# Performance work log

Hardware: AMD Instinct MI355X
Metric: run time of the kernel (lower is better)

The kernel has to match this reference:

```python
import jax, jax.numpy as jnp
import numpy as np
from math import factorial

N_NODES = 20000
N_EDGES = 80000
NUM_GRAPHS = 64
NUM_NEIGHBORS = 3.8
POOL_NODES = 4.0  # num_nodes=4 constant in source forward

# ---------------- real Wigner 3j (e3nn-style, Frobenius norm 1) ----------------

def _w3j_complex(j1, j2, j3, m1, m2, m3):
    if m1 + m2 + m3 != 0:
        return 0.0
    t1 = j2 - m1 - j3; t2 = j1 + m2 - j3; t3 = j1 + j2 - j3
    t4 = j1 - m1; t5 = j2 + m2
    tmin = max(0, t1, t2); tmax = min(t3, t4, t5)
    if tmin > tmax:
        return 0.0
    s = 0.0
    for t in range(tmin, tmax + 1):
        s += (-1.0) ** t / (factorial(t) * factorial(t - t1) * factorial(t - t2)
                            * factorial(t3 - t) * factorial(t4 - t) * factorial(t5 - t))
    tri = (factorial(j1 + j2 - j3) * factorial(j1 - j2 + j3) * factorial(-j1 + j2 + j3)
           / factorial(j1 + j2 + j3 + 1))
    norm = np.sqrt(tri * factorial(j1 + m1) * factorial(j1 - m1) * factorial(j2 + m2)
                   * factorial(j2 - m2) * factorial(j3 + m3) * factorial(j3 - m3))
    return (-1.0) ** (j1 - j2 - m3) * norm * s


def _real_basis(l):
    U = np.zeros((2 * l + 1, 2 * l + 1), dtype=np.complex128)
    U[l, l] = 1.0
    for m in range(1, l + 1):
        U[l + m, l + m] = (-1) ** m / np.sqrt(2.0)
        U[l + m, l - m] = 1.0 / np.sqrt(2.0)
        U[l - m, l - m] = 1j / np.sqrt(2.0)
        U[l - m, l + m] = -1j * (-1) ** m / np.sqrt(2.0)
    return U

_W3J_CACHE = {}

def w3j(l1, l2, l3):
    key = (l1, l2, l3)
    if key not in _W3J_CACHE:
        C = np.zeros((2 * l1 + 1, 2 * l2 + 1, 2 * l3 + 1), dtype=np.complex128)
        for m1 in range(-l1, l1 + 1):
            for m2 in range(-l2, l2 + 1):
                m3 = -(m1 + m2)
                if -l3 <= m3 <= l3:
                    C[m1 + l1, m2 + l2, m3 + l3] = _w3j_complex(l1, l2, l3, m1, m2, m3)
        C = np.einsum('ia,jb,kc,abc->ijk', _real_basis(l1), _real_basis(l2), _real_basis(l3), C)
        C = np.real((-1j) ** (l1 + l2 + l3) * C)
        _W3J_CACHE[key] = jnp.asarray(C, dtype=jnp.float32)
    return _W3J_CACHE[key]

# ---------------- irreps bookkeeping ----------------
SH        = [(1, 0, 1), (1, 1, -1), (1, 2, 1), (1, 3, -1)]            # 1x0e+1x1o+1x2e+1x3o (dim 16)
GATE1_IN  = [(16,0,1),(16,0,-1),(8,0,1),(8,0,-1),(8,0,1),(8,0,-1),(16,1,-1),(16,1,1)]  # dim 160
GATE1_OUT = [(16,0,1),(16,0,1),(16,1,-1),(16,1,1)]                     # dim 128
GATE2_IN  = [(16,0,1),(16,0,-1),(6,0,1),(6,0,-1),(6,0,1),(6,0,-1),(12,1,-1),(12,1,1)]  # dim 128
GATE2_OUT = [(16,0,1),(16,0,1),(12,1,-1),(12,1,1)]                     # dim 104
OUT_FINAL = [(1, 0, 1)]


def slices(irreps):
    out = []; o = 0
    for m, l, p in irreps:
        d = m * (2 * l + 1); out.append((o, o + d)); o += d
    return out


def tp_paths(ir1, ir2, iro):
    paths = []
    for i1, (m1, l1, p1) in enumerate(ir1):
        for i2, (m2, l2, p2) in enumerate(ir2):
            for io, (mo, lo, po) in enumerate(iro):
                if po == p1 * p2 and abs(l1 - l2) <= lo <= l1 + l2:
                    paths.append((i1, i2, io))
    fan = [0] * len(iro)
    for i1, i2, io in paths:
        fan[io] += ir1[i1][0] * ir2[i2][0]
    numel = sum(ir1[i1][0] * ir2[i2][0] * iro[io][0] for i1, i2, io in paths)
    return paths, fan, numel


def tensor_product(x1, x2, weights, ir1, ir2, iro):
    # FullyConnectedTensorProduct, component norm, element path normalization
    paths, fan, numel = tp_paths(ir1, ir2, iro)
    s1, s2 = slices(ir1), slices(ir2)
    E = x1.shape[0]
    out_parts = [jnp.zeros((E, m * (2 * l + 1)), x1.dtype) for m, l, p in iro]
    wofs = 0
    for i1, i2, io in paths:
        m1, l1, _ = ir1[i1]; m2, l2, _ = ir2[i2]; mo, lo, _ = iro[io]
        n = m1 * m2 * mo
        w = weights[:, wofs:wofs + n].reshape(E, m1, m2, mo); wofs += n
        a = x1[:, s1[i1][0]:s1[i1][1]].reshape(E, m1, 2 * l1 + 1)
        b = x2[:, s2[i2][0]:s2[i2][1]].reshape(E, m2, 2 * l2 + 1)
        C = w3j(l1, l2, lo)
        pw = np.sqrt((2 * lo + 1) / fan[io])
        seg = jnp.einsum('eui,evj,ijk,euvw->ewk', a, b, C, w) * pw
        out_parts[io] = out_parts[io] + seg.reshape(E, mo * (2 * lo + 1))
    return jnp.concatenate(out_parts, axis=1)

# ---------------- activations / gate ----------------
_xs = np.linspace(-8.0, 8.0, 100001)
_pdf = np.exp(-0.5 * _xs ** 2) / np.sqrt(2 * np.pi)
TANH_NORM = float(1.0 / np.sqrt(np.sum(np.tanh(_xs) ** 2 * _pdf) * (_xs[1] - _xs[0])))
SQRT2 = float(np.sqrt(2.0))
ACT = {'relu': lambda t: jnp.maximum(t, 0.0) * SQRT2,
       'abs':  lambda t: jnp.abs(t),
       'tanh': lambda t: jnp.tanh(t) * TANH_NORM}


def gate_fn(x, scalars, gates, gated):
    o = 0; outs = []
    for m, a in scalars:
        outs.append(ACT[a](x[:, o:o + m])); o += m
    gv = []
    for m, a in gates:
        gv.append(ACT[a](x[:, o:o + m])); o += m
    g = jnp.concatenate(gv, axis=-1)
    gi = 0
    for m, l in gated:
        d = 2 * l + 1
        feat = x[:, o:o + m * d].reshape(-1, m, d)
        outs.append((feat * g[:, gi:gi + m, None]).reshape(-1, m * d))
        o += m * d; gi += m
    return jnp.concatenate(outs, axis=-1)

# ---------------- edge features ----------------

def sh_component(v):
    # real spherical harmonics l=0..3, 'component' normalization, unit input
    x, y, z = v[:, 0], v[:, 1], v[:, 2]
    s3, s5, s15 = np.sqrt(3.0), np.sqrt(5.0), np.sqrt(15.0)
    s7, s42, s70, s105 = np.sqrt(7.0), np.sqrt(42.0), np.sqrt(70.0), np.sqrt(105.0)
    Y0 = jnp.ones_like(x)[:, None]
    Y1 = jnp.stack([s3 * y, s3 * z, s3 * x], -1)
    Y2 = jnp.stack([s15 * x * y, s15 * y * z, 0.5 * s5 * (3 * z * z - 1.0),
                    s15 * x * z, 0.5 * s15 * (x * x - y * y)], -1)
    Y3 = jnp.stack([0.25 * s70 * y * (3 * x * x - y * y), s105 * x * y * z,
                    0.25 * s42 * y * (5 * z * z - 1.0), 0.5 * s7 * z * (5 * z * z - 3.0),
                    0.25 * s42 * x * (5 * z * z - 1.0), 0.5 * s105 * z * (x * x - y * y),
                    0.25 * s70 * x * (x * x - 3 * y * y)], -1)
    return jnp.concatenate([Y0, Y1, Y2, Y3], -1)  # [E,16]


def soft_one_hot(r):
    # soft_one_hot_linspace(start=0.5,end=2.5,number=3,basis='smooth_finite',cutoff=True)
    values = np.linspace(0.5, 2.5, 5)[1:-1]
    step = values[1] - values[0]
    diff = (r[:, None] - values) / step
    def f(u):
        return jnp.where(u > 0, jnp.exp(-1.0 / jnp.where(u > 0, u, 1.0)), 0.0)
    y = 1.14136 * np.exp(2.0) * f(diff + 1.0) * f(1.0 - diff)
    return y * np.sqrt(3.0)


def fc(x, w1, w2):
    # e3nn FullyConnectedNet([3,256,numel], relu)
    h = jnp.maximum(x @ (w1 / np.sqrt(w1.shape[0])), 0.0) * SQRT2
    return h @ (w2 / np.sqrt(w2.shape[0]))


def convolution(node_feats, edge_src, edge_dst, edge_attr, edge_scalars, w1, w2, ir_in, ir_out, n_nodes):
    weight = fc(edge_scalars, w1, w2)                                   # [E, numel]
    ef = tensor_product(node_feats[edge_src], edge_attr, weight, ir_in, SH, ir_out)
    return jax.ops.segment_sum(ef, edge_dst, num_segments=n_nodes) / np.sqrt(NUM_NEIGHBORS)


def _forward(pos, w1_1, w2_1, w1_2, w2_2, w1_3, w2_3, edge_src, edge_dst, batch):
    N = pos.shape[0]
    vec = pos[edge_src] - pos[edge_dst]
    r = jnp.sqrt(jnp.sum(vec * vec, axis=1) + 1e-12)
    unit = vec / r[:, None]
    edge_attr = sh_component(unit)
    edge_scalars = soft_one_hot(r)
    x = jax.ops.segment_sum(edge_attr, edge_dst, num_segments=N) / np.sqrt(NUM_NEIGHBORS)
    x = convolution(x, edge_src, edge_dst, edge_attr, edge_scalars, w1_1, w2_1, SH, GATE1_IN, N)
    x = gate_fn(x, [(16, 'relu'), (16, 'abs')], [(8, 'relu'), (8, 'tanh'), (8, 'relu'), (8, 'tanh')], [(16, 1), (16, 1)])
    x = convolution(x, edge_src, edge_dst, edge_attr, edge_scalars, w1_2, w2_2, GATE1_OUT, GATE2_IN, N)
    x = gate_fn(x, [(16, 'relu'), (16, 'abs')], [(6, 'relu'), (6, 'tanh'), (6, 'relu'), (6, 'tanh')], [(12, 1), (12, 1)])
    x = convolution(x, edge_src, edge_dst, edge_attr, edge_scalars, w1_3, w2_3, GATE2_OUT, OUT_FINAL, N)
    x = jax.ops.segment_sum(x, batch, num_segments=NUM_GRAPHS) / np.sqrt(POOL_NODES)
    return jax.nn.sigmoid(x)


def setup_inputs():
    key = jax.random.key(0)
    ks = jax.random.split(key, 10)
    pos = jax.random.normal(ks[0], (N_NODES, 3), jnp.float32) * 1.5
    edge_src = jax.random.randint(ks[1], (N_EDGES,), 0, N_NODES)
    edge_dst = jax.random.randint(ks[2], (N_EDGES,), 0, N_NODES)
    batch = jnp.sort(jax.random.randint(ks[3], (N_NODES,), 0, NUM_GRAPHS))
    _, _, n1 = tp_paths(SH, SH, GATE1_IN)
    _, _, n2 = tp_paths(GATE1_OUT, SH, GATE2_IN)
    _, _, n3 = tp_paths(GATE2_OUT, SH, OUT_FINAL)
    w1_1 = jax.random.normal(ks[4], (3, 256), jnp.float32)
    w2_1 = jax.random.normal(ks[5], (256, n1), jnp.float32)
    w1_2 = jax.random.normal(ks[6], (3, 256), jnp.float32)
    w2_2 = jax.random.normal(ks[7], (256, n2), jnp.float32)
    w1_3 = jax.random.normal(ks[8], (3, 256), jnp.float32)
    w2_3 = jax.random.normal(ks[9], (256, n3), jnp.float32)
    return {'pos': pos, 'w1_1': w1_1, 'w2_1': w2_1, 'w1_2': w1_2, 'w2_2': w2_2,
            'w1_3': w1_3, 'w2_3': w2_3, 'edge_src': edge_src, 'edge_dst': edge_dst, 'batch': batch}


def reference(pos, w1_1, w2_1, w1_2, w2_2, w1_3, w2_3, edge_src, edge_dst, batch):
    return _forward(pos, w1_1, w2_1, w1_2, w2_2, w1_3, w2_3, edge_src, edge_dst, batch)
```

## Files before the change

kernel.cpp:

```cpp
#include <hip/hip_runtime.h>
#include <math.h>

#define NNODE 20000
#define NEDGE 80000
#define NGRAPH 64

#define OFF_TANH  656
#define OFF_CNT   660
#define OFF_GSUM  664
#define OFF_HIST  7680
#define OFF_OFFS  9728
#define OFF_CUR   11784
#define OFF_EATTR 14336
#define OFF_RBUF  1294336
#define OFF_EINFO 1374336
#define OFF_X0    1694336
#define OFF_Y1    2014336
#define OFF_Y2    5214336
#define OFF_X1    7774336
#define OFF_X2    10334336
#define OFF_TAB   12414336

#define T000 0
#define T110 1
#define T220 10
#define T330 35
#define T011 84
#define T101 93
#define T111 102
#define T121 129
#define T211 174
#define T231 219
#define T321 324
#define T221 429
#define T331 504

#define INV_SQRT_NEIGH 0.5129891760425771f
#define SQRT2F 1.4142135623730951f

struct TabD { int l1,l2,l3,off; };
constexpr TabD HTABS[13] = {
  {0,0,0,T000},{1,1,0,T110},{2,2,0,T220},{3,3,0,T330},
  {0,1,1,T011},{1,0,1,T101},{1,1,1,T111},{1,2,1,T121},
  {2,1,1,T211},{2,3,1,T231},{3,2,1,T321},{2,2,1,T221},{3,3,1,T331}
};

struct CoreD { short a_off, b_off; short l1,l2,l3; short tab; short coff; short m1; };
struct PathD { short core; short wofs, wend, ooff; short mo, lo; float pw; };

constexpr CoreD HCORES1[13] = {
  {0,0, 0,0,0, T000, 0, 1},
  {0,1, 0,1,1, T011, 1, 1},
  {1,0, 1,0,1, T101, 4, 1},
  {1,1, 1,1,0, T110, 7, 1},
  {1,1, 1,1,1, T111, 8, 1},
  {1,4, 1,2,1, T121, 11, 1},
  {4,1, 2,1,1, T211, 14, 1},
  {4,4, 2,2,0, T220, 17, 1},
  {4,4, 2,2,1, T221, 18, 1},
  {4,9, 2,3,1, T231, 21, 1},
  {9,4, 3,2,1, T321, 24, 1},
  {9,9, 3,3,0, T330, 27, 1},
  {9,9, 3,3,1, T331, 28, 1}
};
#define PWR 0.7071067811865476f
constexpr PathD HPATHS1[21] = {
  {0,  0, 16,  0,16,0,0.5f},
  {0, 16, 24, 32, 8,0,0.5f},
  {0, 24, 32, 48, 8,0,0.5f},
  {1, 32, 48, 64,16,1,PWR},
  {2, 48, 64, 64,16,1,PWR},
  {3, 64, 80,  0,16,0,0.5f},
  {3, 80, 88, 32, 8,0,0.5f},
  {3, 88, 96, 48, 8,0,0.5f},
  {4, 96,112,112,16,1,1.0f},
  {5,112,128, 64,16,1,PWR},
  {6,128,144, 64,16,1,PWR},
  {7,144,160,  0,16,0,0.5f},
  {7,160,168, 32, 8,0,0.5f},
  {7,168,176, 48, 8,0,0.5f},
  {8,176,192,112,16,1,1.0f},
  {9,192,208, 64,16,1,PWR},
  {10,208,224,64,16,1,PWR},
  {11,224,240, 0,16,0,0.5f},
  {11,240,248,32, 8,0,0.5f},
  {11,248,256,48, 8,0,0.5f},
  {12,256,272,112,16,1,1.0f}
};

constexpr CoreD HCORES2[12] = {
  {0,0,  0,0,0, T000, 0,   16},
  {0,1,  0,1,1, T011, 16,  16},
  {16,0, 0,0,0, T000, 64,  16},
  {16,1, 0,1,1, T011, 80,  16},
  {32,0, 1,0,1, T101, 128, 16},
  {32,1, 1,1,0, T110, 176, 16},
  {32,1, 1,1,1, T111, 192, 16},
  {32,4, 1,2,1, T121, 240, 16},
  {80,0, 1,0,1, T101, 288, 16},
  {80,1, 1,1,0, T110, 336, 16},
  {80,1, 1,1,1, T111, 352, 16},
  {80,4, 1,2,1, T121, 400, 16}
};
#define PA 0.14433756729740643f
#define PB 0.25f
#define PC 0.19364916731037085f
constexpr PathD HPATHS2[20] = {
  {0,   0, 256,  0,16,0,PA},
  {0, 256, 352, 32, 6,0,PA},
  {0, 352, 448, 44, 6,0,PA},
  {1, 448, 640, 56,12,1,PC},
  {2, 640, 896,  0,16,0,PA},
  {2, 896, 992, 32, 6,0,PA},
  {2, 992,1088, 44, 6,0,PA},
  {3,1088,1280, 56,12,1,PC},
  {4,1280,1472, 56,12,1,PC},
  {5,1472,1728,  0,16,0,PA},
  {5,1728,1824, 32, 6,0,PA},
  {5,1824,1920, 44, 6,0,PA},
  {6,1920,2112, 92,12,1,PB},
  {7,2112,2304, 56,12,1,PC},
  {8,2304,2496, 92,12,1,PB},
  {9,2496,2752, 16,16,0,PB},
  {9,2752,2848, 38, 6,0,PB},
  {9,2848,2944, 50, 6,0,PB},
  {10,2944,3136,56,12,1,PC},
  {11,3136,3328,92,12,1,PB}
};

constexpr CoreD HCORES3[3] = {
  {0,0,  0,0,0, T000, 0,  16},
  {16,0, 0,0,0, T000, 16, 16},
  {32,1, 1,1,0, T110, 32, 12}
};
#define PD 0.15075567228888181f
constexpr PathD HPATHS3[3] = {
  {0, 0,16, 0,1,0,PD},
  {1,16,32, 0,1,0,PD},
  {2,32,44, 0,1,0,PD}
};

constexpr double FACT[9] = {1.0,1.0,2.0,6.0,24.0,120.0,720.0,5040.0,40320.0};

constexpr double csqrt_(double x){
  if(x<=0.0) return 0.0;
  double g = (x<1.0)? 1.0 : x;
  for(int i=0;i<40;i++) g = 0.5*(g + x/g);
  return g;
}

constexpr double cw3j_(int j1,int j2,int j3,int m1,int m2,int m3){
  if(m1+m2+m3!=0) return 0.0;
  int t1=j2-m1-j3, t2=j1+m2-j3, t3=j1+j2-j3, t4=j1-m1, t5=j2+m2;
  int tmin=t1>0?t1:0; if(t2>tmin) tmin=t2;
  int tmax=t3<t4?t3:t4; if(t5<tmax) tmax=t5;
  if(tmin>tmax) return 0.0;
  double s=0.0;
  for(int t=tmin;t<=tmax;++t){
    double d=FACT[t]*FACT[t-t1]*FACT[t-t2]*FACT[t3-t]*FACT[t4-t]*FACT[t5-t];
    s += ((t&1)? -1.0:1.0)/d;
  }
  double tri=FACT[j1+j2-j3]*FACT[j1-j2+j3]*FACT[-j1+j2+j3]/FACT[j1+j2+j3+1];
  double nrm=csqrt_(tri*FACT[j1+m1]*FACT[j1-m1]*FACT[j2+m2]*FACT[j2-m2]*FACT[j3+m3]*FACT[j3-m3]);
  return (((j1-j2-m3)&1)? -1.0:1.0)*nrm*s;
}

constexpr int curow_(int l,int i,int* a,double* re,double* im){
  const double is2=0.7071067811865475;
  int m=i-l;
  if(m==0){ a[0]=l; re[0]=1.0; im[0]=0.0; return 1; }
  if(m>0){
    a[0]=l+m; re[0]=((m&1)? -is2:is2); im[0]=0.0;
    a[1]=l-m; re[1]=is2; im[1]=0.0; return 2;
  }
  int mm=-m;
  a[0]=l-mm; re[0]=0.0; im[0]=is2;
  a[1]=l+mm; re[1]=0.0; im[1]=((mm&1)? is2:-is2);
  return 2;
}

constexpr float cw3j_elem_(int l1,int l2,int l3,int i,int j,int k){
  int aa[2]={0,0},bb[2]={0,0},cc[2]={0,0};
  double ar[2]={0,0},ai[2]={0,0},br[2]={0,0},bi[2]={0,0},cr[2]={0,0},ci[2]={0,0};
  int na=curow_(l1,i,aa,ar,ai);
  int nb=curow_(l2,j,bb,br,bi);
  int nc=curow_(l3,k,cc,cr,ci);
  double accr=0.0, acci=0.0;
  for(int x=0;x<na;x++)for(int y=0;y<nb;y++)for(int w=0;w<nc;w++){
    double wv=cw3j_(l1,l2,l3, aa[x]-l1, bb[y]-l2, cc[w]-l3);
    if(wv==0.0) continue;
    double pr=ar[x]*br[y]-ai[x]*bi[y];
    double pi=ar[x]*bi[y]+ai[x]*br[y];
    double qr=pr*cr[w]-pi*ci[w];
    double qi=pr*ci[w]+pi*cr[w];
    accr+=qr*wv; acci+=qi*wv;
  }
  int Lm=(l1+l2+l3)&3;
  double res = (Lm==0)? accr : (Lm==1)? acci : (Lm==2)? -accr : -acci;
  return (float)res;
}

struct WApart { float v[429]; };
constexpr WApart gen_wa_(){
  WApart o{};
  for(int t=0;t<11;t++){
    int l1=HTABS[t].l1,l2=HTABS[t].l2,l3=HTABS[t].l3;
    int n2=2*l2+1,n3=2*l3+1;
    int tot=(2*l1+1)*n2*n3;
    for(int z=0;z<tot;z++){
      int i=z/(n2*n3), j=(z/n3)%n2, k=z%n3;
      o.v[HTABS[t].off+z]=cw3j_elem_(l1,l2,l3,i,j,k);
    }
  }
  return o;
}
struct WBpart { float v[222]; };
constexpr WBpart gen_wb_(){
  WBpart o{};
  for(int t=11;t<13;t++){
    int l1=HTABS[t].l1,l2=HTABS[t].l2,l3=HTABS[t].l3;
    int n2=2*l2+1,n3=2*l3+1;
    int tot=(2*l1+1)*n2*n3;
    for(int z=0;z<tot;z++){
      int i=z/(n2*n3), j=(z/n3)%n2, k=z%n3;
      o.v[HTABS[t].off-429+z]=cw3j_elem_(l1,l2,l3,i,j,k);
    }
  }
  return o;
}
constexpr WApart WAC = gen_wa_();
constexpr WBpart WBC = gen_wb_();
struct W3Full { float v[651]; };
constexpr W3Full gen_wfull_(){
  W3Full f{};
  for(int i=0;i<429;i++) f.v[i]=WAC.v[i];
  for(int i=0;i<222;i++) f.v[429+i]=WBC.v[i];
  return f;
}
__constant__ W3Full W3JC = gen_wfull_();

template<int NW> struct PwArr { float v[NW]; };
template<int NW,int NP>
constexpr PwArr<NW> gen_pw_(const PathD (&P)[NP]){
  PwArr<NW> a{};
  for(int p=0;p<NP;p++)
    for(int j=P[p].wofs;j<P[p].wend;j++) a.v[j]=P[p].pw;
  return a;
}
__constant__ PwArr<272>  PWC1 = gen_pw_<272>(HPATHS1);
__constant__ PwArr<3328> PWC2 = gen_pw_<3328>(HPATHS2);
__constant__ PwArr<44>   PWC3 = gen_pw_<44>(HPATHS3);

struct OutSeg { int mult, l; };
constexpr OutSeg OSEG1[8] = {{16,0},{16,0},{8,0},{8,0},{8,0},{8,0},{16,1},{16,1}};
constexpr OutSeg OSEG2[8] = {{16,0},{16,0},{6,0},{6,0},{6,0},{6,0},{12,1},{12,1}};
constexpr OutSeg OSEG3[1] = {{1,0}};

struct Ent2 { int jb, cb, nu; };
template<int NCOL,int NENT,int NW> struct ColMetaT {
  int cidx[NCOL+1];
  int obase[NCOL];
  int n3c[NCOL];
  Ent2 ent[NENT];
  int newj[NW];
};

template<int NCOL,int NENT,int NW,int NSEG,int NP,int NC>
constexpr ColMetaT<NCOL,NENT,NW> gen_colmeta_(const OutSeg (&S)[NSEG], const PathD (&P)[NP], const CoreD (&C)[NC]){
  ColMetaT<NCOL,NENT,NW> m{};
  int col=0, cnt=0, o=0, nb=0;
  for(int s=0;s<NSEG;s++){
    int n3=2*S[s].l+1;
    for(int wc=0;wc<S[s].mult;wc++){
      m.cidx[col]=cnt;
      int ob=o+wc*n3;
      m.obase[col]=ob;
      m.n3c[col]=n3;
      for(int p=0;p<NP;p++){
        PathD pd=P[p];
        int pn3=2*pd.lo+1;
        if(pn3!=n3) continue;
        int rel=ob-pd.ooff;
        if(rel<0||rel>=pd.mo*pn3) continue;
        int w=rel/pn3;
        CoreD cd=C[pd.core];
        int m1=cd.m1;
        m.ent[cnt]=Ent2{nb,(int)cd.coff,m1};
        for(int u=0;u<m1;u++) m.newj[pd.wofs + w + u*pd.mo]=nb+u;
        nb+=m1;
        cnt++;
      }
      col++;
    }
    o+=S[s].mult*n3;
  }
  m.cidx[col]=cnt;
  return m;
}

__constant__ ColMetaT<96,272,272>  CMETA1 = gen_colmeta_<96,272,272>(OSEG1, HPATHS1, HCORES1);
__constant__ ColMetaT<80,208,3328> CMETA2 = gen_colmeta_<80,208,3328>(OSEG2, HPATHS2, HCORES2);
__constant__ ColMetaT< 1,  3,  44> CMETA3 = gen_colmeta_< 1,  3,  44>(OSEG3, HPATHS3, HCORES3);

struct CItem { short aoff, boff, n1, n2, cofs, jstep, woff, pad; };
struct CArr1 { CItem it[31]; };
constexpr CArr1 gen_c1_(){
  CArr1 a{}; int s=0;
  for(int cn=0;cn<13;cn++){
    CoreD cd=HCORES1[cn];
    int n1=2*cd.l1+1,n2=2*cd.l2+1,n3=2*cd.l3+1;
    for(int k=0;k<n3;k++){
      a.it[s]=CItem{cd.a_off,cd.b_off,(short)n1,(short)n2,(short)(cd.tab+k),(short)n3,(short)(cd.coff+k),0};
      s++;
    }
  }
  return a;
}
__constant__ CArr1 CIT1 = gen_c1_();

struct Fam { short b_off, tab, n1, n2, n3, goff; };
constexpr Fam GF2[6]={
  {0,T000,1,1,1,0},{1,T011,1,3,3,1},{0,T101,3,1,3,4},
  {1,T110,3,3,1,13},{1,T111,3,3,3,16},{4,T121,3,5,3,25}};
constexpr Fam GF3[2]={{0,T000,1,1,1,0},{1,T110,3,3,1,1}};
struct CoreG { short fam,a_off,m1,coff; };
constexpr CoreG CG2[12]={
  {0,0,16,0},{1,0,16,16},{0,16,16,64},{1,16,16,80},
  {2,32,16,128},{3,32,16,176},{4,32,16,192},{5,32,16,240},
  {2,80,16,288},{3,80,16,336},{4,80,16,352},{5,80,16,400}};
constexpr CoreG CG3[3]={{0,0,16,0},{0,16,16,16},{1,32,12,32}};

struct GItem { short boff, cofs, n2, jstep; };
template<int NG> struct GArrT { GItem it[NG]; };
template<int NG,int NF>
constexpr GArrT<NG> gen_g_(const Fam (&F)[NF]){
  GArrT<NG> a{}; int s=0;
  for(int f=0;f<NF;f++){
    for(int i=0;i<F[f].n1;i++)for(int k=0;k<F[f].n3;k++){
      a.it[s]=GItem{F[f].b_off,(short)(F[f].tab + i*F[f].n2*F[f].n3 + k),F[f].n2,F[f].n3};
      s++;
    }
  }
  return a;
}
__constant__ GArrT<34> GIT2=gen_g_<34>(GF2);
__constant__ GArrT<4>  GIT3=gen_g_<4>(GF3);

struct OItem { short aoff, gofs, n1, n3, woff, pad; };
template<int NO> struct OArrT { OItem it[NO]; };
template<int NO,int NC,int NF>
constexpr OArrT<NO> gen_o_(const CoreG (&C)[NC], const Fam (&F)[NF]){
  OArrT<NO> a{}; int s=0;
  for(int cn=0;cn<NC;cn++){
    Fam f=F[C[cn].fam];
    for(int k=0;k<f.n3;k++)for(int u=0;u<C[cn].m1;u++){
      a.it[s]=OItem{(short)(C[cn].a_off+u*f.n1),(short)(f.goff+k),f.n1,f.n3,
                    (short)(C[cn].coff+k*C[cn].m1+u),0};
      s++;
    }
  }
  return a;
}
__constant__ OArrT<448> OIT2=gen_o_<448,12,6>(CG2,GF2);
__constant__ OArrT<44>  OIT3=gen_o_<44,3,2>(CG3,GF3);

template<int CNT,int N3,int NCOLS>
__device__ __forceinline__ void apply1_col(const Ent2* __restrict__ ep, const float* __restrict__ T0,
    const float* __restrict__ crb, float fr, float&a0,float&a1,float&a2){
  const float* tja=T0+ep[0].jb;
  float wv[CNT];
  #pragma unroll
  for(int t=0;t<CNT;t++){
    float w0=tja[t], w1=tja[t+NCOLS];
    wv[t]=w0+fr*(w1-w0);
  }
  #pragma unroll
  for(int t=0;t<CNT;t++){
    const float* cr=crb+ep[t].cb;
    a0=fmaf(wv[t],cr[0],a0);
    if constexpr(N3==3){ a1=fmaf(wv[t],cr[1],a1); a2=fmaf(wv[t],cr[2],a2); }
  }
}
__device__ __forceinline__ void apply1_dyn(const Ent2* __restrict__ ep, int cnt, int n3,
    const float* __restrict__ T0, const float* __restrict__ crb, float fr, int NCOLS,
    float&a0,float&a1,float&a2){
  const float* tja=T0+ep[0].jb;
  for(int t=0;t<cnt;t++){
    float w0=tja[t], w1=tja[t+NCOLS];
    float w=w0+fr*(w1-w0);
    const float* cr=crb+ep[t].cb;
    a0=fmaf(w,cr[0],a0);
    if(n3==3){ a1=fmaf(w,cr[1],a1); a2=fmaf(w,cr[2],a2); }
  }
}
template<int CNT,int N3,int NCOLS>
__device__ __forceinline__ void apply2_col(const Ent2* __restrict__ ep, const float* __restrict__ T0,
    const float* __restrict__ crb, float fr, float&a0,float&a1,float&a2){
  #pragma unroll
  for(int t=0;t<CNT;t++){
    const float* cr=crb+ep[t].cb;
    const float* tj=T0+ep[t].jb;
    #pragma unroll
    for(int uu=0;uu<16;uu+=4){
      float4 w0=*(const float4*)(tj+uu);
      float4 w1=*(const float4*)(tj+NCOLS+uu);
      float w;
      if constexpr(N3==1){
        float4 cv=*(const float4*)(cr+uu);
        w=w0.x+fr*(w1.x-w0.x); a0=fmaf(w,cv.x,a0);
        w=w0.y+fr*(w1.y-w0.y); a0=fmaf(w,cv.y,a0);
        w=w0.z+fr*(w1.z-w0.z); a0=fmaf(w,cv.z,a0);
        w=w0.w+fr*(w1.w-w0.w); a0=fmaf(w,cv.w,a0);
      } else {
        float4 c0=*(const float4*)(cr+uu);
        float4 c1=*(const float4*)(cr+16+uu);
        float4 c2=*(const float4*)(cr+32+uu);
        w=w0.x+fr*(w1.x-w0.x); a0=fmaf(w,c0.x,a0); a1=fmaf(w,c1.x,a1); a2=fmaf(w,c2.x,a2);
        w=w0.y+fr*(w1.y-w0.y); a0=fmaf(w,c0.y,a0); a1=fmaf(w,c1.y,a1); a2=fmaf(w,c2.y,a2);
        w=w0.z+fr*(w1.z-w0.z); a0=fmaf(w,c0.z,a0); a1=fmaf(w,c1.z,a1); a2=fmaf(w,c2.z,a2);
        w=w0.w+fr*(w1.w-w0.w); a0=fmaf(w,c0.w,a0); a1=fmaf(w,c1.w,a1); a2=fmaf(w,c2.w,a2);
      }
    }
  }
}
__device__ __forceinline__ void apply2_dyn(const Ent2* __restrict__ ep, int cnt, int n3,
    const float* __restrict__ T0, const float* __restrict__ crb, float fr, int NCOLS,
    float&a0,float&a1,float&a2){
  for(int t=0;t<cnt;t++){
    const float* cr=crb+ep[t].cb;
    const float* tj=T0+ep[t].jb;
    #pragma unroll
    for(int uu=0;uu<16;uu+=4){
      float4 w0=*(const float4*)(tj+uu);
      float4 w1=*(const float4*)(tj+NCOLS+uu);
      float w;
      if(n3==1){
        float4 cv=*(const float4*)(cr+uu);
        w=w0.x+fr*(w1.x-w0.x); a0=fmaf(w,cv.x,a0);
        w=w0.y+fr*(w1.y-w0.y); a0=fmaf(w,cv.y,a0);
        w=w0.z+fr*(w1.z-w0.z); a0=fmaf(w,cv.z,a0);
        w=w0.w+fr*(w1.w-w0.w); a0=fmaf(w,cv.w,a0);
      } else {
        float4 c0=*(const float4*)(cr+uu);
        float4 c1=*(const float4*)(cr+16+uu);
        float4 c2=*(const float4*)(cr+32+uu);
        w=w0.x+fr*(w1.x-w0.x); a0=fmaf(w,c0.x,a0); a1=fmaf(w,c1.x,a1); a2=fmaf(w,c2.x,a2);
        w=w0.y+fr*(w1.y-w0.y); a0=fmaf(w,c0.y,a0); a1=fmaf(w,c1.y,a1); a2=fmaf(w,c2.y,a2);
        w=w0.z+fr*(w1.z-w0.z); a0=fmaf(w,c0.z,a0); a1=fmaf(w,c1.z,a1); a2=fmaf(w,c2.z,a2);
        w=w0.w+fr*(w1.w-w0.w); a0=fmaf(w,c0.w,a0); a1=fmaf(w,c1.w,a1); a2=fmaf(w,c2.w,a2);
      }
    }
  }
}

template<int JT>
__device__ __forceinline__ void table_gemm(const float* __restrict__ W2, float* __restrict__ tab,
    int NCOLS, float scale, const float* __restrict__ PW, const int* __restrict__ NJ,
    int jb, const float (*__restrict__ sh_h)[8], int r0, int R){
  float acc[8][JT];
  #pragma unroll
  for(int k=0;k<8;k++)
    #pragma unroll
    for(int u=0;u<JT;u++) acc[k][u]=0.0f;
  const float* w2p=W2+jb;
  for(int c=0;c<256;c++){
    float w[JT];
    const float* wr=w2p+(size_t)c*NCOLS;
    *(float4*)&w[0]=*(const float4*)wr;
    if constexpr(JT==8) *(float4*)&w[4]=*(const float4*)(wr+4);
    float h[8];
    *(float4*)&h[0]=*(const float4*)&sh_h[c][0];
    *(float4*)&h[4]=*(const float4*)&sh_h[c][4];
    #pragma unroll
    for(int k=0;k<8;k++)
      #pragma unroll
      for(int u=0;u<JT;u++)
        acc[k][u]=fmaf(h[k],w[u],acc[k][u]);
  }
  #pragma unroll
  for(int u=0;u<JT;u++){
    float cs=scale*PW[jb+u];
    int jn=NJ[jb+u];
    #pragma unroll
    for(int k=0;k<8;k++){
      int ri=r0+k;
      if(ri<R) tab[(size_t)ri*NCOLS+jn]=acc[k][u]*cs;
    }
  }
}

__global__ __launch_bounds__(256) void k_tables(
    const float* __restrict__ W1_1, const float* __restrict__ W2_1, float* __restrict__ T1,
    const float* __restrict__ W1_2, const float* __restrict__ W2_2, float* __restrict__ T2,
    const float* __restrict__ W1_3, const float* __restrict__ W2_3, float* __restrict__ T3,
    int R, int NR, float* __restrict__ ws){
  int tid=threadIdx.x;
  int by=blockIdx.y;
  if(by==4){
    if(blockIdx.x!=0) return;
    for(int i=tid;i<(728-OFF_CNT);i+=256) ws[OFF_CNT+i]=0.0f;
    for(int i=tid;i<(13832-OFF_HIST);i+=256) ws[OFF_HIST+i]=0.0f;
    __shared__ double red[256];
    double loc=0.0;
    for(int i=tid;i<=100000;i+=256){
      float x=-8.0f+16.0f*(float)i/100000.0f;
      float th=tanhf(x);
      float pdf=expf(-0.5f*x*x)*0.3989422804014327f;
      loc += (double)(th*th*pdf);
    }
    red[tid]=loc; __syncthreads();
    for(int s=128;s>0;s>>=1){ if(tid<s) red[tid]+=red[tid+s]; __syncthreads(); }
    if(tid==0) ws[OFF_TANH]=(float)(1.0/sqrt(red[0]*(16.0/100000.0)));
    return;
  }
  int conv, jb0;
  const float* W1; const float* W2; float* tab; int NCOLS; float scale;
  if(by==0){ conv=1; jb0=0; W1=W1_1; W2=W2_1; tab=T1; NCOLS=272;  scale=INV_SQRT_NEIGH; }
  else if(by<=2){ conv=2; jb0=(by-1)*2048; W1=W1_2; W2=W2_2; tab=T2; NCOLS=3328; scale=INV_SQRT_NEIGH; }
  else { conv=3; jb0=0; W1=W1_3; W2=W2_3; tab=T3; NCOLS=44;   scale=INV_SQRT_NEIGH*0.5f; }

  __shared__ float sh_h[256][8];
  int r0=blockIdx.x*8;
  {
    int c=tid;
    float wa=W1[c], wb=W1[256+c], wc=W1[512+c];
    const float A=(float)(1.14136*7.38905609893065*1.7320508075688772);
    #pragma unroll
    for(int k=0;k<8;k++){
      int ri=r0+k;
      float r=0.5f+2.0f*(float)ri/(float)NR;
      float sv[3];
      #pragma unroll
      for(int j=0;j<3;j++){
        float v=1.0f+0.5f*(float)j;
        float diff=(r-v)*2.0f;
        float u1=diff+1.0f, u2=1.0f-diff;
        float f1=(u1>0.0f)? expf(-1.0f/u1):0.0f;
        float f2=(u2>0.0f)? expf(-1.0f/u2):0.0f;
        sv[j]=A*f1*f2;
      }
      float hv=sv[0]*wa+sv[1]*wb+sv[2]*wc;
      hv=fmaxf(hv*0.5773502691896258f,0.0f)*(SQRT2F*0.0625f);
      sh_h[c][k]=hv;
    }
  }
  __syncthreads();
  const float* PW=(conv==1)? PWC1.v : (conv==2)? PWC2.v : PWC3.v;
  const int* NJ=(conv==1)? CMETA1.newj : (conv==2)? CMETA2.newj : CMETA3.newj;
  if(conv==3){
    int jb=tid*4;
    if(jb+4<=NCOLS) table_gemm<4>(W2,tab,NCOLS,scale,PW,NJ,jb,sh_h,r0,R);
  } else {
    int jb=jb0+tid*8;
    if(jb+8<=NCOLS) table_gemm<8>(W2,tab,NCOLS,scale,PW,NJ,jb,sh_h,r0,R);
  }
}

__global__ void k_edge(const float* __restrict__ pos, const int* __restrict__ esrc,
                       const int* __restrict__ edst, float* __restrict__ ws, int NR){
  int e = blockIdx.x*256 + threadIdx.x;
  if(e>=NEDGE) return;
  float* eattr=ws+OFF_EATTR;
  float* x0=ws+OFF_X0;
  int s=esrc[e], d=edst[e];
  float x=pos[3*s]-pos[3*d], y=pos[3*s+1]-pos[3*d+1], z=pos[3*s+2]-pos[3*d+2];
  float r=sqrtf(x*x+y*y+z*z+1e-12f);
  float iv=1.0f/r; x*=iv; y*=iv; z*=iv;
  const float s3=1.7320508075688772f, s5=2.2360679774997896f, s15=3.872983346207417f;
  const float s7=2.6457513110645907f, s42=6.48074069840786f, s70=8.366600265340756f, s105=10.246950765959598f;
  float Y[16];
  Y[0]=1.0f;
  Y[1]=s3*y; Y[2]=s3*z; Y[3]=s3*x;
  Y[4]=s15*x*y; Y[5]=s15*y*z; Y[6]=0.5f*s5*(3.0f*z*z-1.0f); Y[7]=s15*x*z; Y[8]=0.5f*s15*(x*x-y*y);
  Y[9]=0.25f*s70*y*(3.0f*x*x-y*y); Y[10]=s105*x*y*z; Y[11]=0.25f*s42*y*(5.0f*z*z-1.0f);
  Y[12]=0.5f*s7*z*(5.0f*z*z-3.0f); Y[13]=0.25f*s42*x*(5.0f*z*z-1.0f);
  Y[14]=0.5f*s105*z*(x*x-y*y); Y[15]=0.25f*s70*x*(x*x-3.0f*y*y);
  float4* ep=(float4*)(eattr+(size_t)e*16);
  ep[0]=make_float4(Y[0],Y[1],Y[2],Y[3]);
  ep[1]=make_float4(Y[4],Y[5],Y[6],Y[7]);
  ep[2]=make_float4(Y[8],Y[9],Y[10],Y[11]);
  ep[3]=make_float4(Y[12],Y[13],Y[14],Y[15]);
  #pragma unroll
  for(int i=0;i<16;i++)
    atomicAdd(&x0[(size_t)d*16+i], Y[i]*INV_SQRT_NEIGH);
  ws[OFF_RBUF+e]=r;
  if(r>0.5f && r<2.5f){
    float t=(r-0.5f)*((float)NR*0.5f);
    int i0=min((int)t, NR-1);
    atomicAdd((int*)(ws+OFF_HIST)+i0, 1);
  }
}

__global__ void k_scan(float* __restrict__ ws, int NR){
  __shared__ int sd[2048];
  int t=threadIdx.x;
  int* hist=(int*)(ws+OFF_HIST);
  int* offs=(int*)(ws+OFF_OFFS);
  int i1=t, i2=t+1024;
  sd[i1]=(i1<NR)? hist[i1]:0;
  sd[i2]=(i2<NR)? hist[i2]:0;
  __syncthreads();
  for(int d=1; d<2048; d<<=1){
    int v1=(i1>=d)? sd[i1-d]:0;
    int v2=(i2>=d)? sd[i2-d]:0;
    __syncthreads();
    sd[i1]+=v1; sd[i2]+=v2;
    __syncthreads();
  }
  if(i1<NR) offs[i1]=(i1==0)?0:sd[i1-1];
  if(i2<NR) offs[i2]=sd[i2-1];
  if(t==0){ offs[NR]=sd[NR-1]; *((int*)(ws+OFF_CNT))=sd[NR-1]; }
}

__global__ void k_scatter(const int* __restrict__ esrc, const int* __restrict__ edst,
                          float* __restrict__ ws, int NR){
  int e=blockIdx.x*256+threadIdx.x;
  if(e>=NEDGE) return;
  float r=ws[OFF_RBUF+e];
  if(!(r>0.5f && r<2.5f)) return;
  float t=(r-0.5f)*((float)NR*0.5f);
  int i0=min((int)t, NR-1);
  int* offs=(int*)(ws+OFF_OFFS);
  int* cur=(int*)(ws+OFF_CUR);
  int p=offs[i0]+atomicAdd(&cur[i0],1);
  int4 v; v.x=esrc[e]; v.y=edst[e]; v.z=e; v.w=__float_as_int(t);
  ((int4*)(ws+OFF_EINFO))[p]=v;
}

template<int CONV,int DY,int D_IN,int D_OUT,int CSTRIDE,int NCOL,int NCOLS,bool FINAL>
__global__ __launch_bounds__(256,4) void k_conv(
    const float* __restrict__ xin, const float* __restrict__ TAB,
    float* __restrict__ yout, const int* __restrict__ batchp,
    float* __restrict__ ws, int NR)
{
  constexpr int APAD = D_IN+4;
  constexpr int NGP  = (CONV==2)?36:4;
  constexpr int YST  = (CONV==3)?132:4;
  constexpr int NGV  = (CONV==2)?32:((CONV==3)?24:1);
  __shared__ float sh_a[8][APAD];
  __shared__ float sh_b[8][20];
  __shared__ float sh_core[8][CSTRIDE];
  __shared__ float sh_g[8][NGP];
  __shared__ float sh_gv[8][NGV];
  __shared__ float sh_y[8][YST];
  __shared__ float sh_red[8];
  __shared__ int sh_src[8], sh_dst[8], sh_eid[8];
  __shared__ float sh_t[8];

  int tid=threadIdx.x;
  int nact=*(const int*)(ws+OFF_CNT);
  int base=blockIdx.x*8;
  if(base>=nact) return;
  int ne=min(8, nact-base);

  if(tid<8){
    int src=0,dst=0,eid=-1; float tv=0.0f;
    if(tid<ne){
      int4 v=((const int4*)(ws+OFF_EINFO))[base+tid];
      src=v.x; dst=v.y; eid=v.z; tv=__int_as_float(v.w);
    }
    sh_src[tid]=src; sh_dst[tid]=dst; sh_eid[tid]=eid; sh_t[tid]=tv;
    if constexpr(CONV==3) sh_red[tid]=0.0f;
  }
  __syncthreads();

  if(tid<32){
    int idx=tid>>2, c4=tid&3;
    int eid=sh_eid[idx];
    float4 v=make_float4(0.f,0.f,0.f,0.f);
    if(eid>=0) v=((const float4*)(ws+OFF_EATTR+(size_t)eid*16))[c4];
    *(float4*)&sh_b[idx][c4*4]=v;
  }
  if constexpr(CONV==1){
    if(tid>=32 && tid<64){
      int t2=tid-32; int idx=t2>>2, c4=t2&3;
      float4 v=make_float4(0.f,0.f,0.f,0.f);
      if(sh_eid[idx]>=0) v=((const float4*)(xin+(size_t)sh_src[idx]*16))[c4];
      *(float4*)&sh_a[idx][c4*4]=v;
    }
  } else {
    constexpr int YQ=DY/4;
    for(int z=tid; z<8*YQ; z+=256){
      int idx=z/YQ, c4=z-idx*YQ;
      float4 v=make_float4(0.f,0.f,0.f,0.f);
      if(sh_eid[idx]>=0) v=((const float4*)(xin+(size_t)sh_src[idx]*DY))[c4];
      if constexpr(CONV==2) *(float4*)&sh_core[idx][c4*4]=v;
      else                  *(float4*)&sh_y[idx][c4*4]=v;
    }
  }
  __syncthreads();

  if constexpr(CONV==1){
    constexpr int NIT=31;
    for(int z=tid; z<8*NIT; z+=256){
      int idx=z/NIT, rem=z-idx*NIT;
      CItem it=CIT1.it[rem];
      float acc=0.0f;
      for(int i=0;i<it.n1;i++){
        float av=sh_a[idx][it.aoff+i];
        int cb=it.cofs + i*it.n2*it.jstep;
        for(int j=0;j<it.n2;j++)
          acc += av*sh_b[idx][it.boff+j]*W3JC.v[cb + j*it.jstep];
      }
      sh_core[idx][it.woff]=acc;
    }
    __syncthreads();
  } else {
    float TN=ws[OFF_TANH];
    for(int z=tid; z<8*NGV; z+=256){
      int idx=z/NGV, m=z-idx*NGV;
      const float* yr=(CONV==2)? &sh_core[idx][0] : &sh_y[idx][0];
      float u=yr[32+m];
      bool th=(CONV==2)? (((m>>3)&1)!=0) : (((m/6)&1)!=0);
      sh_gv[idx][m]= th? tanhf(u)*TN : fmaxf(u,0.0f)*SQRT2F;
    }
    constexpr int NG=(CONV==2)?34:4;
    for(int z=tid; z<8*NG; z+=256){
      int idx=z/NG, rem=z-idx*NG;
      GItem it=(CONV==2)? GIT2.it[rem] : GIT3.it[rem];
      float acc=0.0f;
      for(int j=0;j<it.n2;j++)
        acc += sh_b[idx][it.boff+j]*W3JC.v[it.cofs + j*it.jstep];
      sh_g[idx][rem]=acc;
    }
    __syncthreads();
    for(int z=tid; z<8*D_IN; z+=256){
      int idx=z/D_IN, o=z-idx*D_IN;
      const float* yr=(CONV==2)? &sh_core[idx][0] : &sh_y[idx][0];
      float val;
      if(o<16) val=fmaxf(yr[o],0.0f)*SQRT2F;
      else if(o<32) val=fabsf(yr[o]);
      else {
        if constexpr(CONV==2){
          int gi=(o<80)? (o-32)/3 : 16+(o-80)/3;
          val=yr[o+32]*sh_gv[idx][gi];
        } else {
          int gi=(o<68)? (o-32)/3 : 12+(o-68)/3;
          val=yr[o+24]*sh_gv[idx][gi];
        }
      }
      sh_a[idx][o]=val;
    }
    __syncthreads();
    constexpr int NO=(CONV==2)?448:44;
    for(int z=tid; z<8*NO; z+=256){
      int idx=z/NO, rem=z-idx*NO;
      OItem it=(CONV==2)? OIT2.it[rem] : OIT3.it[rem];
      float acc=0.0f;
      #pragma unroll 3
      for(int i=0;i<it.n1;i++)
        acc += sh_a[idx][it.aoff+i]*sh_g[idx][it.gofs + i*it.n3];
      sh_core[idx][it.woff]=acc;
    }
    __syncthreads();
  }

  if constexpr(CONV==3){
    if(tid<88){
      int e3=tid&7, c=tid>>3;
      float tv=sh_t[e3];
      int i0=min((int)tv, NR-1);
      float fr=tv-(float)i0;
      const float* tj=TAB+(size_t)i0*NCOLS + c*4;
      float4 w0=*(const float4*)tj;
      float4 w1=*(const float4*)(tj+NCOLS);
      float4 cv=*(const float4*)(&sh_core[e3][c*4]);
      float p;
      p  = (w0.x+fr*(w1.x-w0.x))*cv.x;
      p += (w0.y+fr*(w1.y-w0.y))*cv.y;
      p += (w0.z+fr*(w1.z-w0.z))*cv.z;
      p += (w0.w+fr*(w1.w-w0.w))*cv.w;
      atomicAdd(&sh_red[e3], p);
    }
    __syncthreads();
    if(tid<ne) atomicAdd(&ws[OFF_GSUM+batchp[sh_dst[tid]]], sh_red[tid]);
  } else {
    int e=tid&7;
    float tv=sh_t[e];
    int i0=min((int)tv, NR-1);
    float fr=tv-(float)i0;
    const float* T0=TAB+(size_t)i0*NCOLS;
    const float* crb=&sh_core[e][0];
    int dstv=sh_dst[e];
    bool act=(e<ne);

    for(int q=tid; q<8*NCOL; q+=256){
      int c=q>>3;
      int s0,s1,ob,n3;
      const Ent2* entp;
      if constexpr(CONV==1){ s0=CMETA1.cidx[c]; s1=CMETA1.cidx[c+1]; ob=CMETA1.obase[c]; n3=CMETA1.n3c[c]; entp=CMETA1.ent; }
      else                 { s0=CMETA2.cidx[c]; s1=CMETA2.cidx[c+1]; ob=CMETA2.obase[c]; n3=CMETA2.n3c[c]; entp=CMETA2.ent; }
      int cnt=s1-s0;
      if(!cnt) continue;
      float a0=0.0f,a1=0.0f,a2=0.0f;
      const Ent2* ep=entp+s0;
      if constexpr(CONV==1){
        if(n3==1){
          switch(cnt){
            case 4: apply1_col<4,1,272>(ep,T0,crb,fr,a0,a1,a2); break;
            default: apply1_dyn(ep,cnt,1,T0,crb,fr,272,a0,a1,a2); break;
          }
        } else {
          switch(cnt){
            case 6: apply1_col<6,3,272>(ep,T0,crb,fr,a0,a1,a2); break;
            case 3: apply1_col<3,3,272>(ep,T0,crb,fr,a0,a1,a2); break;
            default: apply1_dyn(ep,cnt,3,T0,crb,fr,272,a0,a1,a2); break;
          }
        }
      } else {
        if(n3==1){
          switch(cnt){
            case 3: apply2_col<3,1,3328>(ep,T0,crb,fr,a0,a1,a2); break;
            case 1: apply2_col<1,1,3328>(ep,T0,crb,fr,a0,a1,a2); break;
            default: apply2_dyn(ep,cnt,1,T0,crb,fr,3328,a0,a1,a2); break;
          }
        } else {
          switch(cnt){
            case 5: apply2_col<5,3,3328>(ep,T0,crb,fr,a0,a1,a2); break;
            case 3: apply2_col<3,3,3328>(ep,T0,crb,fr,a0,a1,a2); break;
            default: apply2_dyn(ep,cnt,3,T0,crb,fr,3328,a0,a1,a2); break;
          }
        }
      }
      if(act){
        float* yp=&yout[(size_t)dstv*D_OUT+ob];
        atomicAdd(yp, a0);
        if(n3==3){ atomicAdd(yp+1, a1); atomicAdd(yp+2, a2); }
      }
    }
  }
}

__global__ void k_sig(const float* __restrict__ ws, float* __restrict__ out){
  int g=threadIdx.x;
  if(g<NGRAPH){
    float v=ws[OFF_GSUM+g];
    out[g]=1.0f/(1.0f+expf(-v));
  }
}

extern "C" void kernel_launch(void* const* d_in, const int* in_sizes, int n_in,
                              void* d_out, int out_size, void* d_ws, size_t ws_size,
                              hipStream_t stream){
  const float* pos =(const float*)d_in[0];
  const float* w1_1=(const float*)d_in[1];
  const float* w2_1=(const float*)d_in[2];
  const float* w1_2=(const float*)d_in[3];
  const float* w2_2=(const float*)d_in[4];
  const float* w1_3=(const float*)d_in[5];
  const float* w2_3=(const float*)d_in[6];
  const int* esrc=(const int*)d_in[7];
  const int* edst=(const int*)d_in[8];
  const int* batch=(const int*)d_in[9];
  float* ws=(float*)d_ws;
  float* out=(float*)d_out;

  long availRows = ((long)(ws_size/4) - (long)OFF_TAB)/3644L;
  int R = (availRows < 1025L)? (int)availRows : 1025;
  if(R < 9) R = 9;
  int NR = R-1;
  float* TAB1 = ws + OFF_TAB;
  float* TAB2 = TAB1 + (size_t)R*272;
  float* TAB3 = TAB2 + (size_t)R*3328;

  hipMemsetAsync(ws+OFF_X0, 0, (size_t)(OFF_X1-OFF_X0)*sizeof(float), stream);

  k_tables<<<dim3((R+7)/8,5),256,0,stream>>>(
      w1_1,w2_1,TAB1, w1_2,w2_2,TAB2, w1_3,w2_3,TAB3, R,NR, ws);
  k_edge<<<(NEDGE+255)/256,256,0,stream>>>(pos, esrc, edst, ws, NR);
  k_scan<<<1,1024,0,stream>>>(ws, NR);
  k_scatter<<<(NEDGE+255)/256,256,0,stream>>>(esrc, edst, ws, NR);

  k_conv<1, 16, 16,160, 33, 96, 272,false><<<(NEDGE+7)/8,256,0,stream>>>(
      ws+OFF_X0, TAB1, ws+OFF_Y1, batch, ws, NR);

  k_conv<2,160,128,128,452, 80,3328,false><<<(NEDGE+7)/8,256,0,stream>>>(
      ws+OFF_Y1, TAB2, ws+OFF_Y2, batch, ws, NR);

  k_conv<3,128,104,  1, 68,  1, 44,true ><<<(NEDGE+7)/8,256,0,stream>>>(
      ws+OFF_Y2, TAB3, nullptr, batch, ws, NR);

  k_sig<<<1,64,0,stream>>>(ws, out);
}
```

Before: 383.2 us.

## Widen table-GEMM blocks to 512 threads with 4-column tiles and prefetch W2 rows

Switches the k_tables blocks from 256 to 512 threads, each computing a 4-column tile instead of 8, so the conv2 tables get twice as many threads working in parallel. The inner GEMM loop now handles two rows of c per iteration and loads the next W2 rows into registers ahead of use (software prefetch). The large conv2 block-rows are also reordered to blockIdx.y 0 and 1 so they are scheduled first. The trade-off is less register reuse of the h values per W2 load and more threads contending for the same shared sh_h data; the extra 256 threads sit idle during the sh_h setup.

```diff
diff --git a/kernel.cpp b/kernel.cpp
--- a/kernel.cpp
+++ b/kernel.cpp
@@ -463,19 +463,40 @@
     #pragma unroll
     for(int u=0;u<JT;u++) acc[k][u]=0.0f;
   const float* w2p=W2+jb;
-  for(int c=0;c<256;c++){
-    float w[JT];
-    const float* wr=w2p+(size_t)c*NCOLS;
-    *(float4*)&w[0]=*(const float4*)wr;
-    if constexpr(JT==8) *(float4*)&w[4]=*(const float4*)(wr+4);
-    float h[8];
-    *(float4*)&h[0]=*(const float4*)&sh_h[c][0];
-    *(float4*)&h[4]=*(const float4*)&sh_h[c][4];
+  float w0[JT], w1[JT];
+  *(float4*)&w0[0]=*(const float4*)(w2p);
+  *(float4*)&w1[0]=*(const float4*)(w2p+NCOLS);
+  if constexpr(JT==8){
+    *(float4*)&w0[4]=*(const float4*)(w2p+4);
+    *(float4*)&w1[4]=*(const float4*)(w2p+NCOLS+4);
+  }
+  for(int c=0;c<256;c+=2){
+    int cp0=(c+2<256)?(c+2):255;
+    int cp1=(c+3<256)?(c+3):255;
+    float n0[JT], n1[JT];
+    *(float4*)&n0[0]=*(const float4*)(w2p+(size_t)cp0*NCOLS);
+    *(float4*)&n1[0]=*(const float4*)(w2p+(size_t)cp1*NCOLS);
+    if constexpr(JT==8){
+      *(float4*)&n0[4]=*(const float4*)(w2p+(size_t)cp0*NCOLS+4);
+      *(float4*)&n1[4]=*(const float4*)(w2p+(size_t)cp1*NCOLS+4);
+    }
+    float h0[8], h1[8];
+    *(float4*)&h0[0]=*(const float4*)&sh_h[c][0];
+    *(float4*)&h0[4]=*(const float4*)&sh_h[c][4];
+    *(float4*)&h1[0]=*(const float4*)&sh_h[c+1][0];
+    *(float4*)&h1[4]=*(const float4*)&sh_h[c+1][4];
     #pragma unroll
     for(int k=0;k<8;k++)
       #pragma unroll
       for(int u=0;u<JT;u++)
-        acc[k][u]=fmaf(h[k],w[u],acc[k][u]);
+        acc[k][u]=fmaf(h0[k],w0[u],acc[k][u]);
+    #pragma unroll
+    for(int k=0;k<8;k++)
+      #pragma unroll
+      for(int u=0;u<JT;u++)
+        acc[k][u]=fmaf(h1[k],w1[u],acc[k][u]);
+    #pragma unroll
+    for(int u=0;u<JT;u++){ w0[u]=n0[u]; w1[u]=n1[u]; }
   }
   #pragma unroll
   for(int u=0;u<JT;u++){
@@ -489,7 +510,7 @@
   }
 }
 
-__global__ __launch_bounds__(256) void k_tables(
+__global__ __launch_bounds__(512) void k_tables(
     const float* __restrict__ W1_1, const float* __restrict__ W2_1, float* __restrict__ T1,
     const float* __restrict__ W1_2, const float* __restrict__ W2_2, float* __restrict__ T2,
     const float* __restrict__ W1_3, const float* __restrict__ W2_3, float* __restrict__ T3,
@@ -498,30 +519,31 @@
   int by=blockIdx.y;
   if(by==4){
     if(blockIdx.x!=0) return;
-    for(int i=tid;i<(728-OFF_CNT);i+=256) ws[OFF_CNT+i]=0.0f;
-    for(int i=tid;i<(13832-OFF_HIST);i+=256) ws[OFF_HIST+i]=0.0f;
-    __shared__ double red[256];
+    for(int i=tid;i<(728-OFF_CNT);i+=512) ws[OFF_CNT+i]=0.0f;
+    for(int i=tid;i<(13832-OFF_HIST);i+=512) ws[OFF_HIST+i]=0.0f;
+    __shared__ double red[512];
     double loc=0.0;
-    for(int i=tid;i<=100000;i+=256){
+    for(int i=tid;i<=100000;i+=512){
       float x=-8.0f+16.0f*(float)i/100000.0f;
       float th=tanhf(x);
       float pdf=expf(-0.5f*x*x)*0.3989422804014327f;
       loc += (double)(th*th*pdf);
     }
     red[tid]=loc; __syncthreads();
-    for(int s=128;s>0;s>>=1){ if(tid<s) red[tid]+=red[tid+s]; __syncthreads(); }
+    for(int s=256;s>0;s>>=1){ if(tid<s) red[tid]+=red[tid+s]; __syncthreads(); }
     if(tid==0) ws[OFF_TANH]=(float)(1.0/sqrt(red[0]*(16.0/100000.0)));
     return;
   }
   int conv, jb0;
   const float* W1; const float* W2; float* tab; int NCOLS; float scale;
-  if(by==0){ conv=1; jb0=0; W1=W1_1; W2=W2_1; tab=T1; NCOLS=272;  scale=INV_SQRT_NEIGH; }
-  else if(by<=2){ conv=2; jb0=(by-1)*2048; W1=W1_2; W2=W2_2; tab=T2; NCOLS=3328; scale=INV_SQRT_NEIGH; }
+  if(by==0){ conv=2; jb0=0;    W1=W1_2; W2=W2_2; tab=T2; NCOLS=3328; scale=INV_SQRT_NEIGH; }
+  else if(by==1){ conv=2; jb0=2048; W1=W1_2; W2=W2_2; tab=T2; NCOLS=3328; scale=INV_SQRT_NEIGH; }
+  else if(by==2){ conv=1; jb0=0; W1=W1_1; W2=W2_1; tab=T1; NCOLS=272;  scale=INV_SQRT_NEIGH; }
   else { conv=3; jb0=0; W1=W1_3; W2=W2_3; tab=T3; NCOLS=44;   scale=INV_SQRT_NEIGH*0.5f; }
 
   __shared__ float sh_h[256][8];
   int r0=blockIdx.x*8;
-  {
+  if(tid<256){
     int c=tid;
     float wa=W1[c], wb=W1[256+c], wc=W1[512+c];
     const float A=(float)(1.14136*7.38905609893065*1.7320508075688772);
@@ -547,13 +569,9 @@
   __syncthreads();
   const float* PW=(conv==1)? PWC1.v : (conv==2)? PWC2.v : PWC3.v;
   const int* NJ=(conv==1)? CMETA1.newj : (conv==2)? CMETA2.newj : CMETA3.newj;
-  if(conv==3){
-    int jb=tid*4;
-    if(jb+4<=NCOLS) table_gemm<4>(W2,tab,NCOLS,scale,PW,NJ,jb,sh_h,r0,R);
-  } else {
-    int jb=jb0+tid*8;
-    if(jb+8<=NCOLS) table_gemm<8>(W2,tab,NCOLS,scale,PW,NJ,jb,sh_h,r0,R);
-  }
+  int jb=jb0+tid*4;
+  if(jb+4<=((conv==2)? ((jb0==0)?2048:NCOLS) : NCOLS))
+    table_gemm<4>(W2,tab,NCOLS,scale,PW,NJ,jb,sh_h,r0,R);
 }
 
 __global__ void k_edge(const float* __restrict__ pos, const int* __restrict__ esrc,
@@ -865,7 +883,7 @@
 
   hipMemsetAsync(ws+OFF_X0, 0, (size_t)(OFF_X1-OFF_X0)*sizeof(float), stream);
 
-  k_tables<<<dim3((R+7)/8,5),256,0,stream>>>(
+  k_tables<<<dim3((R+7)/8,5),512,0,stream>>>(
       w1_1,w2_1,TAB1, w1_2,w2_2,TAB2, w1_3,w2_3,TAB3, R,NR, ws);
   k_edge<<<(NEDGE+255)/256,256,0,stream>>>(pos, esrc, edst, ws, NR);
   k_scan<<<1,1024,0,stream>>>(ws, NR);
```

Result: no change. 376.0 us (-1.9%).
